# Kernel optimization log

Measured on AMD Instinct MI355X. Metric: run time of the kernel, lower is better.

## Reference

```python
import jax, jax.numpy as jnp
import numpy as np

B, S, D, H, DFF = 2, 2048, 2048, 16, 8192
DH = D // H
EPS = 1e-5


def _layer_norm(x, g, b):
    mu = jnp.mean(x, axis=-1, keepdims=True)
    var = jnp.mean(jnp.square(x - mu), axis=-1, keepdims=True)
    return (x - mu) * jax.lax.rsqrt(var + EPS) * g + b


def setup_inputs() -> dict:
    key = jax.random.key(0)
    ks = jax.random.split(key, 12)
    sc = 0.02
    inp = {
        "x": jax.random.normal(ks[0], (B, S, D), dtype=jnp.float32),
        # attention projections, stored [in, out] (torch Linear weight transposed)
        "wq": jax.random.normal(ks[1], (D, D), dtype=jnp.float32) * sc,
        "bq": jnp.zeros((D,), jnp.float32),
        "wk": jax.random.normal(ks[2], (D, D), dtype=jnp.float32) * sc,
        "bk": jnp.zeros((D,), jnp.float32),
        "wv": jax.random.normal(ks[3], (D, D), dtype=jnp.float32) * sc,
        "bv": jnp.zeros((D,), jnp.float32),
        "wo": jax.random.normal(ks[4], (D, D), dtype=jnp.float32) * sc,
        "bo": jnp.zeros((D,), jnp.float32),
        "ln1_g": jnp.ones((D,), jnp.float32),
        "ln1_b": jnp.zeros((D,), jnp.float32),
        # feed-forward
        "w1": jax.random.normal(ks[5], (D, DFF), dtype=jnp.float32) * sc,
        "b1": jnp.zeros((DFF,), jnp.float32),
        "w2": jax.random.normal(ks[6], (DFF, D), dtype=jnp.float32) * sc,
        "b2": jnp.zeros((D,), jnp.float32),
        "ln2_g": jnp.ones((D,), jnp.float32),
        "ln2_b": jnp.zeros((D,), jnp.float32),
    }
    return inp


def reference(x, wq, bq, wk, bk, wv, bv, wo, bo, ln1_g, ln1_b,
              w1, b1, w2, b2, ln2_g, ln2_b):
    # ---- MultiHeadAttentionBlock: x + MHA(LN(x)) ----
    h = _layer_norm(x, ln1_g, ln1_b)                      # [B,S,D]
    q = (h @ wq + bq).reshape(B, S, H, DH).transpose(0, 2, 1, 3)  # [B,H,S,DH]
    k = (h @ wk + bk).reshape(B, S, H, DH).transpose(0, 2, 1, 3)
    v = (h @ wv + bv).reshape(B, S, H, DH).transpose(0, 2, 1, 3)

    # faithful to source: scale by sqrt(d_dim), NOT sqrt(head_dim)
    scores = jnp.einsum("bhqd,bhkd->bhqk", q, k) / np.sqrt(D).astype(np.float32)
    # faithful triu/transpose masking (softmax sees raw zeros, not -inf)
    t = jnp.triu(scores).swapaxes(-2, -1)                 # [B,H,S,S]
    s = jax.nn.softmax(t, axis=-2)
    r = jnp.triu(s).swapaxes(-2, -1)
    attn = jnp.einsum("bhqk,bhkd->bhqd", r, v)            # [B,H,S,DH]
    attn = attn.transpose(0, 2, 1, 3).reshape(B, S, D)
    x = x + attn @ wo + bo

    # ---- FeedForwardBlock: x + FF(LN(x)), dropout rate 0 ----
    h2 = _layer_norm(x, ln2_g, ln2_b)
    ff = jax.nn.relu(h2 @ w1 + b1) @ w2 + b2
    return x + ff
```

## Files before the change

kernel.cpp:

```cpp
#include <hip/hip_runtime.h>


typedef unsigned short ushort_t;
typedef unsigned int   uint32;
typedef __attribute__((ext_vector_type(8))) short    short8;
typedef __attribute__((ext_vector_type(8))) ushort_t ushort8;
typedef __attribute__((ext_vector_type(4))) float    f32x4;

#define BDIM   2
#define SEQ    2048
#define DMODEL 2048
#define NHEAD  16
#define DHEAD  128
#define DFFN   8192
#define MROWS  (BDIM*SEQ)
#define LDQKV  6144

#define GPTR(p) (const __attribute__((address_space(1))) void*)((const void*)(p))
#define SPTR(p) (__attribute__((address_space(3))) void*)((void*)(p))

__device__ __forceinline__ float bf2f(ushort_t u) {
  union { uint32 i; float f; } c; c.i = ((uint32)u) << 16; return c.f;
}
__device__ __forceinline__ ushort_t f2bf(float f) {
  union { float f; uint32 i; } c; c.f = f;
  uint32 u = c.i;
  return (ushort_t)((u + 0x7fffu + ((u >> 16) & 1u)) >> 16);
}

__global__ __launch_bounds__(256) void transpose_f32_bf16_kern(
    const float* __restrict__ W, ushort_t* __restrict__ Wt, int K, int N)
{
  __shared__ float tile[32][33];
  const int nb = blockIdx.x * 32, kb = blockIdx.y * 32;
  const int tx = threadIdx.x & 31, ty = threadIdx.x >> 5;
#pragma unroll
  for (int j = 0; j < 32; j += 8)
    tile[ty + j][tx] = W[(size_t)(kb + ty + j) * N + nb + tx];
  __syncthreads();
#pragma unroll
  for (int j = 0; j < 32; j += 8)
    Wt[(size_t)(nb + ty + j) * K + kb + tx] = f2bf(tile[tx][ty + j]);
}

__global__ __launch_bounds__(256) void bias_concat_kern(
    const float* __restrict__ a, const float* __restrict__ b,
    const float* __restrict__ c, float* __restrict__ o)
{
  const int i = blockIdx.x * 256 + threadIdx.x;
  o[i] = (i < 2048) ? a[i] : ((i < 4096) ? b[i - 2048] : c[i - 4096]);
}

__global__ __launch_bounds__(256) void ln_kern(
    const float* __restrict__ X, const float* __restrict__ G,
    const float* __restrict__ Bb, ushort_t* __restrict__ Out)
{
  const int row = blockIdx.x, tid = threadIdx.x;
  const float* xr = X + (size_t)row * DMODEL;
  float4 v0 = ((const float4*)xr)[tid * 2];
  float4 v1 = ((const float4*)xr)[tid * 2 + 1];
  float s  = v0.x + v0.y + v0.z + v0.w + v1.x + v1.y + v1.z + v1.w;
  float ss = v0.x*v0.x + v0.y*v0.y + v0.z*v0.z + v0.w*v0.w
           + v1.x*v1.x + v1.y*v1.y + v1.z*v1.z + v1.w*v1.w;
#pragma unroll
  for (int off = 32; off > 0; off >>= 1) {
    s  += __shfl_down(s, off);
    ss += __shfl_down(ss, off);
  }
  __shared__ float rs[4], rss[4];
  __shared__ float sh_mu, sh_rst;
  const int wv = tid >> 6;
  if ((tid & 63) == 0) { rs[wv] = s; rss[wv] = ss; }
  __syncthreads();
  if (tid == 0) {
    float S1 = rs[0] + rs[1] + rs[2] + rs[3];
    float S2 = rss[0] + rss[1] + rss[2] + rss[3];
    float mu = S1 * (1.f / DMODEL);
    float var = S2 * (1.f / DMODEL) - mu * mu;
    sh_mu = mu;
    sh_rst = rsqrtf(var + 1e-5f);
  }
  __syncthreads();
  const float mu = sh_mu, rst = sh_rst;
  float4 g0 = ((const float4*)G)[tid * 2];
  float4 g1 = ((const float4*)G)[tid * 2 + 1];
  float4 b0 = ((const float4*)Bb)[tid * 2];
  float4 b1 = ((const float4*)Bb)[tid * 2 + 1];
  ushort8 o;
  o[0] = f2bf((v0.x - mu) * rst * g0.x + b0.x);
  o[1] = f2bf((v0.y - mu) * rst * g0.y + b0.y);
  o[2] = f2bf((v0.z - mu) * rst * g0.z + b0.z);
  o[3] = f2bf((v0.w - mu) * rst * g0.w + b0.w);
  o[4] = f2bf((v1.x - mu) * rst * g1.x + b1.x);
  o[5] = f2bf((v1.y - mu) * rst * g1.y + b1.y);
  o[6] = f2bf((v1.z - mu) * rst * g1.z + b1.z);
  o[7] = f2bf((v1.w - mu) * rst * g1.w + b1.w);
  *(ushort8*)(Out + (size_t)row * DMODEL + tid * 8) = o;
}

template<int OUT_BF16, int RELU, int RESID>
__global__ __launch_bounds__(512) void gemm_pipe_kern(
    const ushort_t* __restrict__ A, const ushort_t* __restrict__ Bt,
    const float* __restrict__ bias, const float* __restrict__ resid,
    void* __restrict__ Cout, int M, int N, int K)
{
  __shared__ ushort_t sA[3 * 128 * 64];
  __shared__ ushort_t sB[3 * 256 * 64];

  const int tid = threadIdx.x;
  const int nM  = gridDim.y;
  const int nwg = gridDim.x * nM;
  const int bid = blockIdx.y * gridDim.x + blockIdx.x;
  const int cpx = nwg >> 3;
  const int swz = (bid & 7) * cpx + (bid >> 3);
  const int m0 = (swz % nM) * 128;
  const int n0 = (swz / nM) * 256;

  const int l  = tid & 63, w = tid >> 6;
  const int lr = l & 15, lg = l >> 4;
  const int wr = w >> 2, wc = w & 3;

  const int srow  = tid >> 3;
  const int schunk = (tid & 7) ^ (srow & 7);
  const ushort_t* Asrc = A  + (size_t)(m0 + srow) * K + schunk * 8;
  const ushort_t* Bsrc = Bt + (size_t)(n0 + srow) * K + schunk * 8;
  ushort_t* sAd = sA + tid * 8;
  ushort_t* sBd = sB + tid * 8;

  const int rxk  = lr & 7;
  const int aoff = (wr * 64 + lr) * 64;
  const int boff = (wc * 64 + lr) * 64;

  f32x4 acc[4][4] = {};
  const int T = K >> 6;

#define STAGE_A(d, kt, r) __builtin_amdgcn_global_load_lds( \
    GPTR(Asrc + (size_t)(kt) * 64 + (size_t)(r) * 64 * K), \
    SPTR(sAd + (d) * 8192 + (r) * 4096), 16, 0, 0)
#define STAGE_B(d, kt, r) __builtin_amdgcn_global_load_lds( \
    GPTR(Bsrc + (size_t)(kt) * 64 + (size_t)(r) * 64 * K), \
    SPTR(sBd + (d) * 16384 + (r) * 4096), 16, 0, 0)

  STAGE_A(0, 0, 0); STAGE_A(0, 0, 1);
  STAGE_B(0, 0, 0); STAGE_B(0, 0, 1); STAGE_B(0, 0, 2); STAGE_B(0, 0, 3);
  STAGE_A(1, 1, 0); STAGE_A(1, 1, 1);
  STAGE_B(1, 1, 0); STAGE_B(1, 1, 1); STAGE_B(1, 1, 2); STAGE_B(1, 1, 3);
  asm volatile("s_waitcnt vmcnt(6)" ::: "memory");
  __builtin_amdgcn_s_barrier();
  __builtin_amdgcn_sched_barrier(0);

  int cur = 0;
  for (int t = 0; t < T; ++t) {
    const int nx = (cur == 0) ? 2 : cur - 1;
    const ushort_t* pA = sA + cur * 8192;
    const ushort_t* pB = sB + cur * 16384;
    const bool pf = (t + 2 < T);

    short8 a0 = *(const short8*)(pA + aoff +    0 + ((0 ^ rxk)) * 8 + (lg ^ 0) * 0);
    a0 = *(const short8*)(pA + aoff +    0 + ((lg ^ rxk)) * 8);
    short8 a1 = *(const short8*)(pA + aoff + 1024 + ((lg ^ rxk)) * 8);
    short8 a2 = *(const short8*)(pA + aoff + 2048 + ((lg ^ rxk)) * 8);
    short8 a3 = *(const short8*)(pA + aoff + 3072 + ((lg ^ rxk)) * 8);
    short8 b0 = *(const short8*)(pB + boff +    0 + ((lg ^ rxk)) * 8);
    short8 b1 = *(const short8*)(pB + boff + 1024 + ((lg ^ rxk)) * 8);
    short8 b2 = *(const short8*)(pB + boff + 2048 + ((lg ^ rxk)) * 8);
    short8 b3 = *(const short8*)(pB + boff + 3072 + ((lg ^ rxk)) * 8);
    if (pf) { STAGE_A(nx, t + 2, 0); STAGE_A(nx, t + 2, 1); STAGE_B(nx, t + 2, 0); }
    __builtin_amdgcn_s_barrier();
    asm volatile("s_waitcnt lgkmcnt(0)" ::: "memory");
    __builtin_amdgcn_sched_barrier(0);
    __builtin_amdgcn_s_setprio(1);
    acc[0][0] = __builtin_amdgcn_mfma_f32_16x16x32_bf16(a0, b0, acc[0][0], 0, 0, 0);
    acc[1][0] = __builtin_amdgcn_mfma_f32_16x16x32_bf16(a1, b0, acc[1][0], 0, 0, 0);
    acc[2][0] = __builtin_amdgcn_mfma_f32_16x16x32_bf16(a2, b0, acc[2][0], 0, 0, 0);
    acc[3][0] = __builtin_amdgcn_mfma_f32_16x16x32_bf16(a3, b0, acc[3][0], 0, 0, 0);
    acc[0][1] = __builtin_amdgcn_mfma_f32_16x16x32_bf16(a0, b1, acc[0][1], 0, 0, 0);
    acc[1][1] = __builtin_amdgcn_mfma_f32_16x16x32_bf16(a1, b1, acc[1][1], 0, 0, 0);
    acc[2][1] = __builtin_amdgcn_mfma_f32_16x16x32_bf16(a2, b1, acc[2][1], 0, 0, 0);
    acc[3][1] = __builtin_amdgcn_mfma_f32_16x16x32_bf16(a3, b1, acc[3][1], 0, 0, 0);
    acc[0][2] = __builtin_amdgcn_mfma_f32_16x16x32_bf16(a0, b2, acc[0][2], 0, 0, 0);
    acc[1][2] = __builtin_amdgcn_mfma_f32_16x16x32_bf16(a1, b2, acc[1][2], 0, 0, 0);
    acc[2][2] = __builtin_amdgcn_mfma_f32_16x16x32_bf16(a2, b2, acc[2][2], 0, 0, 0);
    acc[3][2] = __builtin_amdgcn_mfma_f32_16x16x32_bf16(a3, b2, acc[3][2], 0, 0, 0);
    acc[0][3] = __builtin_amdgcn_mfma_f32_16x16x32_bf16(a0, b3, acc[0][3], 0, 0, 0);
    acc[1][3] = __builtin_amdgcn_mfma_f32_16x16x32_bf16(a1, b3, acc[1][3], 0, 0, 0);
    acc[2][3] = __builtin_amdgcn_mfma_f32_16x16x32_bf16(a2, b3, acc[2][3], 0, 0, 0);
    acc[3][3] = __builtin_amdgcn_mfma_f32_16x16x32_bf16(a3, b3, acc[3][3], 0, 0, 0);
    __builtin_amdgcn_s_setprio(0);
    __builtin_amdgcn_s_barrier();

    a0 = *(const short8*)(pA + aoff +    0 + (((4 + lg) ^ rxk)) * 8);
    a1 = *(const short8*)(pA + aoff + 1024 + (((4 + lg) ^ rxk)) * 8);
    a2 = *(const short8*)(pA + aoff + 2048 + (((4 + lg) ^ rxk)) * 8);
    a3 = *(const short8*)(pA + aoff + 3072 + (((4 + lg) ^ rxk)) * 8);
    b0 = *(const short8*)(pB + boff +    0 + (((4 + lg) ^ rxk)) * 8);
    b1 = *(const short8*)(pB + boff + 1024 + (((4 + lg) ^ rxk)) * 8);
    b2 = *(const short8*)(pB + boff + 2048 + (((4 + lg) ^ rxk)) * 8);
    b3 = *(const short8*)(pB + boff + 3072 + (((4 + lg) ^ rxk)) * 8);
    if (pf) { STAGE_B(nx, t + 2, 1); STAGE_B(nx, t + 2, 2); STAGE_B(nx, t + 2, 3); }
    __builtin_amdgcn_s_barrier();
    asm volatile("s_waitcnt lgkmcnt(0)" ::: "memory");
    __builtin_amdgcn_sched_barrier(0);
    __builtin_amdgcn_s_setprio(1);
    acc[0][0] = __builtin_amdgcn_mfma_f32_16x16x32_bf16(a0, b0, acc[0][0], 0, 0, 0);
    acc[1][0] = __builtin_amdgcn_mfma_f32_16x16x32_bf16(a1, b0, acc[1][0], 0, 0, 0);
    acc[2][0] = __builtin_amdgcn_mfma_f32_16x16x32_bf16(a2, b0, acc[2][0], 0, 0, 0);
    acc[3][0] = __builtin_amdgcn_mfma_f32_16x16x32_bf16(a3, b0, acc[3][0], 0, 0, 0);
    acc[0][1] = __builtin_amdgcn_mfma_f32_16x16x32_bf16(a0, b1, acc[0][1], 0, 0, 0);
    acc[1][1] = __builtin_amdgcn_mfma_f32_16x16x32_bf16(a1, b1, acc[1][1], 0, 0, 0);
    acc[2][1] = __builtin_amdgcn_mfma_f32_16x16x32_bf16(a2, b1, acc[2][1], 0, 0, 0);
    acc[3][1] = __builtin_amdgcn_mfma_f32_16x16x32_bf16(a3, b1, acc[3][1], 0, 0, 0);
    acc[0][2] = __builtin_amdgcn_mfma_f32_16x16x32_bf16(a0, b2, acc[0][2], 0, 0, 0);
    acc[1][2] = __builtin_amdgcn_mfma_f32_16x16x32_bf16(a1, b2, acc[1][2], 0, 0, 0);
    acc[2][2] = __builtin_amdgcn_mfma_f32_16x16x32_bf16(a2, b2, acc[2][2], 0, 0, 0);
    acc[3][2] = __builtin_amdgcn_mfma_f32_16x16x32_bf16(a3, b2, acc[3][2], 0, 0, 0);
    acc[0][3] = __builtin_amdgcn_mfma_f32_16x16x32_bf16(a0, b3, acc[0][3], 0, 0, 0);
    acc[1][3] = __builtin_amdgcn_mfma_f32_16x16x32_bf16(a1, b3, acc[1][3], 0, 0, 0);
    acc[2][3] = __builtin_amdgcn_mfma_f32_16x16x32_bf16(a2, b3, acc[2][3], 0, 0, 0);
    acc[3][3] = __builtin_amdgcn_mfma_f32_16x16x32_bf16(a3, b3, acc[3][3], 0, 0, 0);
    __builtin_amdgcn_s_setprio(0);
    if (pf) { asm volatile("s_waitcnt vmcnt(6)" ::: "memory"); }
    else    { asm volatile("s_waitcnt vmcnt(0)" ::: "memory"); }
    __builtin_amdgcn_s_barrier();
    __builtin_amdgcn_sched_barrier(0);
    cur = (cur == 2) ? 0 : cur + 1;
  }
#undef STAGE_A
#undef STAGE_B

#pragma unroll
  for (int mi = 0; mi < 4; ++mi) {
#pragma unroll
    for (int ni = 0; ni < 4; ++ni) {
      const int gn = n0 + wc * 64 + ni * 16 + lr;
      const float bvv = bias[gn];
#pragma unroll
      for (int j = 0; j < 4; ++j) {
        const int gm = m0 + wr * 64 + mi * 16 + lg * 4 + j;
        float v = acc[mi][ni][j] + bvv;
        if (RESID) v += resid[(size_t)gm * N + gn];
        if (RELU) v = fmaxf(v, 0.f);
        if (OUT_BF16) ((ushort_t*)Cout)[(size_t)gm * N + gn] = f2bf(v);
        else          ((float*)Cout)[(size_t)gm * N + gn] = v;
      }
    }
  }
}

__global__ __launch_bounds__(256) void attn_stats_kern(
    const ushort_t* __restrict__ Q, const ushort_t* __restrict__ Kb,
    float* __restrict__ E, float* __restrict__ DG, int ld)
{
  __shared__ ushort_t Ksm[64 * 128];
  const int qb = blockIdx.x;
  const int bh = blockIdx.y;
  const int b = bh >> 4, h = bh & 15;
  const int tid = threadIdx.x;
  const int l = tid & 63, w = tid >> 6;
  const int lr = l & 15, lg = l >> 4;

  const int qrow0 = qb * 64 + w * 16;

  const size_t qoff = (size_t)(b * SEQ + qrow0 + lr) * ld + h * DHEAD + lg * 8;
  short8 af[4];
#pragma unroll
  for (int c = 0; c < 4; ++c) af[c] = *(const short8*)(Q + qoff + c * 32);

  const int srow_b = w * 16 + (l >> 4);
  const ushort_t* Kg = Kb + (size_t)b * SEQ * ld + (size_t)h * DHEAD;
  ushort_t* Sbase = Ksm + w * 2048;

  f32x4 sume = {0.f, 0.f, 0.f, 0.f};
  f32x4 dge  = {0.f, 0.f, 0.f, 0.f};
  const float scale = 0.0220970869120796f;
  const int rx = lr & 7;

  for (int kc = qb; kc < 32; ++kc) {
    __syncthreads();
#pragma unroll
    for (int c = 0; c < 4; ++c) {
      const int row = srow_b + c * 4;
      const int g = (l & 15) ^ (row & 7);
      __builtin_amdgcn_global_load_lds(
          GPTR(Kg + (size_t)(kc * 64 + row) * ld + g * 8),
          SPTR(Sbase + c * 512), 16, 0, 0);
    }
    __syncthreads();

    const int ks0 = (kc == qb) ? w : 0;
    for (int ks = ks0; ks < 4; ++ks) {
      short8 bfr[4];
#pragma unroll
      for (int c = 0; c < 4; ++c)
        bfr[c] = *(const short8*)(Ksm + (ks * 16 + lr) * 128 + ((lg + c * 4) ^ rx) * 8);
      f32x4 sc = {0.f, 0.f, 0.f, 0.f};
      sc = __builtin_amdgcn_mfma_f32_16x16x32_bf16(af[0], bfr[0], sc, 0, 0, 0);
      sc = __builtin_amdgcn_mfma_f32_16x16x32_bf16(af[1], bfr[1], sc, 0, 0, 0);
      sc = __builtin_amdgcn_mfma_f32_16x16x32_bf16(af[2], bfr[2], sc, 0, 0, 0);
      sc = __builtin_amdgcn_mfma_f32_16x16x32_bf16(af[3], bfr[3], sc, 0, 0, 0);
      if (kc == qb && ks == w) {
        const int ki = kc * 64 + ks * 16 + lr;
#pragma unroll
        for (int j = 0; j < 4; ++j) {
          const int qi = qrow0 + lg * 4 + j;
          if (ki >= qi) {
            float e = __expf(sc[j] * scale);
            sume[j] += e;
            if (ki == qi) dge[j] += e;
          }
        }
      } else {
#pragma unroll
        for (int j = 0; j < 4; ++j)
          sume[j] += __expf(sc[j] * scale);
      }
    }
  }

#pragma unroll
  for (int j = 0; j < 4; ++j) {
#pragma unroll
    for (int off = 1; off < 16; off <<= 1) {
      sume[j] += __shfl_xor(sume[j], off);
      dge[j]  += __shfl_xor(dge[j], off);
    }
  }
  if (lr == 0) {
#pragma unroll
    for (int j = 0; j < 4; ++j) {
      E[(size_t)bh * SEQ + qrow0 + lg * 4 + j]  = sume[j];
      DG[(size_t)bh * SEQ + qrow0 + lg * 4 + j] = dge[j];
    }
  }
}

__global__ __launch_bounds__(128) void vchunk_kern(
    const ushort_t* __restrict__ V, float* __restrict__ CS, int ld)
{
  const int c = blockIdx.x, bh = blockIdx.y;
  const int b = bh >> 4, h = bh & 15;
  const int dh = threadIdx.x;
  const ushort_t* vp = V + (size_t)(b * SEQ + c * 64) * ld + h * DHEAD + dh;
  float s = 0.f;
  for (int i = 0; i < 64; ++i) s += bf2f(vp[(size_t)i * ld]);
  CS[((size_t)bh * 32 + c) * 128 + dh] = s;
}

__global__ __launch_bounds__(128) void attn_combine_kern(
    const ushort_t* __restrict__ V, const float* __restrict__ CS,
    const float* __restrict__ E, const float* __restrict__ DG,
    ushort_t* __restrict__ Attn, int ldv)
{
  const int c = blockIdx.x, bh = blockIdx.y;
  const int b = bh >> 4, h = bh & 15;
  const int dh = threadIdx.x;
  float prefix = 0.f;
  for (int cc = 0; cc < c; ++cc) prefix += CS[((size_t)bh * 32 + cc) * 128 + dh];
  const ushort_t* vp = V + (size_t)(b * SEQ + c * 64) * ldv + h * DHEAD + dh;
  ushort_t* ap = Attn + (size_t)(b * SEQ + c * 64) * DMODEL + h * DHEAD + dh;
  const int qb = c * 64;
  for (int i = 0; i < 64; ++i) {
    const int qq = qb + i;
    const float denom = (float)qq + E[(size_t)bh * SEQ + qq];
    const float de = DG[(size_t)bh * SEQ + qq];
    const float vv = bf2f(vp[(size_t)i * ldv]);
    ap[(size_t)i * DMODEL] = f2bf((prefix + de * vv) / denom);
    prefix += vv;
  }
}

extern "C" void kernel_launch(void* const* d_in, const int* in_sizes, int n_in,
                              void* d_out, int out_size, void* d_ws, size_t ws_size,
                              hipStream_t stream)
{
  const float* x    = (const float*)d_in[0];
  const float* wq   = (const float*)d_in[1];
  const float* bq   = (const float*)d_in[2];
  const float* wk   = (const float*)d_in[3];
  const float* bk   = (const float*)d_in[4];
  const float* wv   = (const float*)d_in[5];
  const float* bv   = (const float*)d_in[6];
  const float* wo   = (const float*)d_in[7];
  const float* bo   = (const float*)d_in[8];
  const float* ln1g = (const float*)d_in[9];
  const float* ln1b = (const float*)d_in[10];
  const float* w1   = (const float*)d_in[11];
  const float* b1   = (const float*)d_in[12];
  const float* w2   = (const float*)d_in[13];
  const float* b2   = (const float*)d_in[14];
  const float* ln2g = (const float*)d_in[15];
  const float* ln2b = (const float*)d_in[16];
  float* out = (float*)d_out;

  char* ws = (char*)d_ws;
  ushort_t* W1T  = (ushort_t*)(ws + 0);
  ushort_t* W2T  = (ushort_t*)(ws + 33554432);
  ushort_t* WOT  = (ushort_t*)(ws + 67108864);
  float*    X2   = (float*)   (ws + 75497472);
  float*    Bcat = (float*)   (ws + 75497472);
  ushort_t* Hb   = (ushort_t*)(ws + 109051904);
  ushort_t* F1   = (ushort_t*)(ws + 125829120);
  ushort_t* WQKV = (ushort_t*)(ws + 125829120);
  ushort_t* QKVb = (ushort_t*)(ws + 150994944);
  float*    Eb   = (float*)   (ws + 201326592);
  float*    DGb  = (float*)   (ws + 201588736);
  float*    CSb  = (float*)   (ws + 201850880);

  transpose_f32_bf16_kern<<<dim3(64, 64),  256, 0, stream>>>(wq, WQKV,                 2048, 2048);
  transpose_f32_bf16_kern<<<dim3(64, 64),  256, 0, stream>>>(wk, WQKV + 2048 * 2048,   2048, 2048);
  transpose_f32_bf16_kern<<<dim3(64, 64),  256, 0, stream>>>(wv, WQKV + 2 * 2048 * 2048, 2048, 2048);
  transpose_f32_bf16_kern<<<dim3(64, 64),  256, 0, stream>>>(wo, WOT, 2048, 2048);
  transpose_f32_bf16_kern<<<dim3(256, 64), 256, 0, stream>>>(w1, W1T, 2048, 8192);
  transpose_f32_bf16_kern<<<dim3(64, 256), 256, 0, stream>>>(w2, W2T, 8192, 2048);
  bias_concat_kern<<<24, 256, 0, stream>>>(bq, bk, bv, Bcat);

  ln_kern<<<MROWS, 256, 0, stream>>>(x, ln1g, ln1b, Hb);

  gemm_pipe_kern<1, 0, 0><<<dim3(24, 32), 512, 0, stream>>>(Hb, WQKV, Bcat, nullptr, QKVb, MROWS, LDQKV, DMODEL);

  attn_stats_kern<<<dim3(32, 32), 256, 0, stream>>>(QKVb, QKVb + 2048, Eb, DGb, LDQKV);

  vchunk_kern<<<dim3(32, 32), 128, 0, stream>>>(QKVb + 4096, CSb, LDQKV);
  attn_combine_kern<<<dim3(32, 32), 128, 0, stream>>>(QKVb + 4096, CSb, Eb, DGb, Hb, LDQKV);

  gemm_pipe_kern<0, 0, 1><<<dim3(8, 32), 512, 0, stream>>>(Hb, WOT, bo, x, X2, MROWS, DMODEL, DMODEL);

  ln_kern<<<MROWS, 256, 0, stream>>>(X2, ln2g, ln2b, Hb);

  gemm_pipe_kern<1, 1, 0><<<dim3(32, 32), 512, 0, stream>>>(Hb, W1T, b1, nullptr, F1, MROWS, DFFN, DMODEL);

  gemm_pipe_kern<0, 0, 1><<<dim3(8, 32), 512, 0, stream>>>(F1, W2T, b2, X2, out, MROWS, DMODEL, DFFN);
}
```

Baseline: 719.6 us.

## Use 256x256 GEMM tiles with split-K partials and a combine kernel

Replaces the 128x256 triple-buffered GEMM with a 256x256 tile kernel that stages K in 32-wide half-slots across four LDS buffers, holding 8x4 accumulators per wave. The two N=2048 GEMMs (output projection and FFN down-projection) are split across K into two bf16 partial buffers, and a new combine kernel adds the partials, bias and residual. The goal is more data reuse per tile and enough workgroups on the narrow GEMMs to fill the device. In exchange it adds an extra elementwise pass, rounds partial sums to bf16, and raises register pressure.

After: 654.2 us. -9.1%, faster.

```diff
diff --git a/kernel.cpp b/kernel.cpp
--- a/kernel.cpp
+++ b/kernel.cpp
@@ -98,14 +98,14 @@
   *(ushort8*)(Out + (size_t)row * DMODEL + tid * 8) = o;
 }
 
-template<int OUT_BF16, int RELU, int RESID>
-__global__ __launch_bounds__(512) void gemm_pipe_kern(
+template<int OUT, int RELU, int RESID, int KDIV>
+__global__ __launch_bounds__(512, 2) void gemm8_kern(
     const ushort_t* __restrict__ A, const ushort_t* __restrict__ Bt,
     const float* __restrict__ bias, const float* __restrict__ resid,
     void* __restrict__ Cout, int M, int N, int K)
 {
-  __shared__ ushort_t sA[3 * 128 * 64];
-  __shared__ ushort_t sB[3 * 256 * 64];
+  __shared__ ushort_t sA[4 * 8192];
+  __shared__ ushort_t sB[4 * 8192];
 
   const int tid = threadIdx.x;
   const int nM  = gridDim.y;
@@ -113,138 +113,212 @@
   const int bid = blockIdx.y * gridDim.x + blockIdx.x;
   const int cpx = nwg >> 3;
   const int swz = (bid & 7) * cpx + (bid >> 3);
-  const int m0 = (swz % nM) * 128;
+  const int m0 = (swz % nM) * 256;
   const int n0 = (swz / nM) * 256;
 
-  const int l  = tid & 63, w = tid >> 6;
+  const int Keff = K / KDIV;
+  const int k0 = (KDIV > 1) ? blockIdx.z * Keff : 0;
+  const int T = Keff >> 6;
+
+  const int l = tid & 63, w = tid >> 6;
   const int lr = l & 15, lg = l >> 4;
   const int wr = w >> 2, wc = w & 3;
 
-  const int srow  = tid >> 3;
-  const int schunk = (tid & 7) ^ (srow & 7);
-  const ushort_t* Asrc = A  + (size_t)(m0 + srow) * K + schunk * 8;
-  const ushort_t* Bsrc = Bt + (size_t)(n0 + srow) * K + schunk * 8;
-  ushort_t* sAd = sA + tid * 8;
-  ushort_t* sBd = sB + tid * 8;
-
-  const int rxk  = lr & 7;
-  const int aoff = (wr * 64 + lr) * 64;
-  const int boff = (wc * 64 + lr) * 64;
-
-  f32x4 acc[4][4] = {};
-  const int T = K >> 6;
-
-#define STAGE_A(d, kt, r) __builtin_amdgcn_global_load_lds( \
-    GPTR(Asrc + (size_t)(kt) * 64 + (size_t)(r) * 64 * K), \
-    SPTR(sAd + (d) * 8192 + (r) * 4096), 16, 0, 0)
-#define STAGE_B(d, kt, r) __builtin_amdgcn_global_load_lds( \
-    GPTR(Bsrc + (size_t)(kt) * 64 + (size_t)(r) * 64 * K), \
-    SPTR(sBd + (d) * 16384 + (r) * 4096), 16, 0, 0)
-
-  STAGE_A(0, 0, 0); STAGE_A(0, 0, 1);
-  STAGE_B(0, 0, 0); STAGE_B(0, 0, 1); STAGE_B(0, 0, 2); STAGE_B(0, 0, 3);
-  STAGE_A(1, 1, 0); STAGE_A(1, 1, 1);
-  STAGE_B(1, 1, 0); STAGE_B(1, 1, 1); STAGE_B(1, 1, 2); STAGE_B(1, 1, 3);
-  asm volatile("s_waitcnt vmcnt(6)" ::: "memory");
+  const int xch   = (lg ^ ((lr >> 1) & 3)) * 8;
+  const int abase = (wr * 128 + lr) * 32 + xch;
+  const int bbase = (wc * 64  + lr) * 32 + xch;
+
+  const int sr = tid >> 2;
+  const int sg = ((tid & 3) ^ ((tid >> 3) & 3)) * 8;
+  const ushort_t* Asrc = A  + (size_t)(m0 + sr) * K + k0 + sg;
+  const ushort_t* Bsrc = Bt + (size_t)(n0 + sr) * K + k0 + sg;
+  ushort_t* dA = sA + tid * 8;
+  ushort_t* dB = sB + tid * 8;
+
+#define SA_(slot, kt, kk, r) __builtin_amdgcn_global_load_lds( \
+    GPTR(Asrc + (size_t)(r) * 128 * K + (kt) * 64 + (kk) * 32), \
+    SPTR(dA + (slot) * 8192 + (r) * 4096), 16, 0, 0)
+#define SB_(slot, kt, kk, r) __builtin_amdgcn_global_load_lds( \
+    GPTR(Bsrc + (size_t)(r) * 128 * K + (kt) * 64 + (kk) * 32), \
+    SPTR(dB + (slot) * 8192 + (r) * 4096), 16, 0, 0)
+
+  f32x4 acc[8][4] = {};
+
+  SA_(0, 0, 0, 0); SA_(0, 0, 0, 1); SB_(0, 0, 0, 0); SB_(0, 0, 0, 1);
+  SA_(1, 0, 1, 0); SA_(1, 0, 1, 1); SB_(1, 0, 1, 0); SB_(1, 0, 1, 1);
+  SA_(2, 1, 0, 0); SA_(2, 1, 0, 1); SB_(2, 1, 0, 0); SB_(2, 1, 0, 1);
+  asm volatile("s_waitcnt vmcnt(8)" ::: "memory");
   __builtin_amdgcn_s_barrier();
-  __builtin_amdgcn_sched_barrier(0);
-
-  int cur = 0;
+
   for (int t = 0; t < T; ++t) {
-    const int nx = (cur == 0) ? 2 : cur - 1;
-    const ushort_t* pA = sA + cur * 8192;
-    const ushort_t* pB = sB + cur * 16384;
-    const bool pf = (t + 2 < T);
-
-    short8 a0 = *(const short8*)(pA + aoff +    0 + ((0 ^ rxk)) * 8 + (lg ^ 0) * 0);
-    a0 = *(const short8*)(pA + aoff +    0 + ((lg ^ rxk)) * 8);
-    short8 a1 = *(const short8*)(pA + aoff + 1024 + ((lg ^ rxk)) * 8);
-    short8 a2 = *(const short8*)(pA + aoff + 2048 + ((lg ^ rxk)) * 8);
-    short8 a3 = *(const short8*)(pA + aoff + 3072 + ((lg ^ rxk)) * 8);
-    short8 b0 = *(const short8*)(pB + boff +    0 + ((lg ^ rxk)) * 8);
-    short8 b1 = *(const short8*)(pB + boff + 1024 + ((lg ^ rxk)) * 8);
-    short8 b2 = *(const short8*)(pB + boff + 2048 + ((lg ^ rxk)) * 8);
-    short8 b3 = *(const short8*)(pB + boff + 3072 + ((lg ^ rxk)) * 8);
-    if (pf) { STAGE_A(nx, t + 2, 0); STAGE_A(nx, t + 2, 1); STAGE_B(nx, t + 2, 0); }
-    __builtin_amdgcn_s_barrier();
-    asm volatile("s_waitcnt lgkmcnt(0)" ::: "memory");
-    __builtin_amdgcn_sched_barrier(0);
+    const int c = t & 1;
+    const ushort_t* A0 = sA + (c * 2 + 0) * 8192;
+    const ushort_t* B0 = sB + (c * 2 + 0) * 8192;
+    const ushort_t* A1 = sA + (c * 2 + 1) * 8192;
+    const ushort_t* B1 = sB + (c * 2 + 1) * 8192;
+    const int s1 = (c ^ 1) * 2 + 1;
+    const int s0 = c * 2;
+    const bool pf1 = (t + 1 < T), pf0 = (t + 2 < T);
+
+    short8 a0, a1, a2, a3, b0, b1, b2, b3;
+
+    b0 = *(const short8*)(B0 + bbase);
+    b1 = *(const short8*)(B0 + bbase + 512);
+    b2 = *(const short8*)(B0 + bbase + 1024);
+    b3 = *(const short8*)(B0 + bbase + 1536);
+    a0 = *(const short8*)(A0 + abase);
+    a1 = *(const short8*)(A0 + abase + 512);
+    a2 = *(const short8*)(A0 + abase + 1024);
+    a3 = *(const short8*)(A0 + abase + 1536);
+    if (pf1) { SA_(s1, t + 1, 1, 0); SA_(s1, t + 1, 1, 1); }
     __builtin_amdgcn_s_setprio(1);
     acc[0][0] = __builtin_amdgcn_mfma_f32_16x16x32_bf16(a0, b0, acc[0][0], 0, 0, 0);
+    acc[0][1] = __builtin_amdgcn_mfma_f32_16x16x32_bf16(a0, b1, acc[0][1], 0, 0, 0);
+    acc[0][2] = __builtin_amdgcn_mfma_f32_16x16x32_bf16(a0, b2, acc[0][2], 0, 0, 0);
+    acc[0][3] = __builtin_amdgcn_mfma_f32_16x16x32_bf16(a0, b3, acc[0][3], 0, 0, 0);
     acc[1][0] = __builtin_amdgcn_mfma_f32_16x16x32_bf16(a1, b0, acc[1][0], 0, 0, 0);
+    acc[1][1] = __builtin_amdgcn_mfma_f32_16x16x32_bf16(a1, b1, acc[1][1], 0, 0, 0);
+    acc[1][2] = __builtin_amdgcn_mfma_f32_16x16x32_bf16(a1, b2, acc[1][2], 0, 0, 0);
+    acc[1][3] = __builtin_amdgcn_mfma_f32_16x16x32_bf16(a1, b3, acc[1][3], 0, 0, 0);
     acc[2][0] = __builtin_amdgcn_mfma_f32_16x16x32_bf16(a2, b0, acc[2][0], 0, 0, 0);
+    acc[2][1] = __builtin_amdgcn_mfma_f32_16x16x32_bf16(a2, b1, acc[2][1], 0, 0, 0);
+    acc[2][2] = __builtin_amdgcn_mfma_f32_16x16x32_bf16(a2, b2, acc[2][2], 0, 0, 0);
+    acc[2][3] = __builtin_amdgcn_mfma_f32_16x16x32_bf16(a2, b3, acc[2][3], 0, 0, 0);
     acc[3][0] = __builtin_amdgcn_mfma_f32_16x16x32_bf16(a3, b0, acc[3][0], 0, 0, 0);
-    acc[0][1] = __builtin_amdgcn_mfma_f32_16x16x32_bf16(a0, b1, acc[0][1], 0, 0, 0);
-    acc[1][1] = __builtin_amdgcn_mfma_f32_16x16x32_bf16(a1, b1, acc[1][1], 0, 0, 0);
-    acc[2][1] = __builtin_amdgcn_mfma_f32_16x16x32_bf16(a2, b1, acc[2][1], 0, 0, 0);
     acc[3][1] = __builtin_amdgcn_mfma_f32_16x16x32_bf16(a3, b1, acc[3][1], 0, 0, 0);
-    acc[0][2] = __builtin_amdgcn_mfma_f32_16x16x32_bf16(a0, b2, acc[0][2], 0, 0, 0);
-    acc[1][2] = __builtin_amdgcn_mfma_f32_16x16x32_bf16(a1, b2, acc[1][2], 0, 0, 0);
-    acc[2][2] = __builtin_amdgcn_mfma_f32_16x16x32_bf16(a2, b2, acc[2][2], 0, 0, 0);
     acc[3][2] = __builtin_amdgcn_mfma_f32_16x16x32_bf16(a3, b2, acc[3][2], 0, 0, 0);
-    acc[0][3] = __builtin_amdgcn_mfma_f32_16x16x32_bf16(a0, b3, acc[0][3], 0, 0, 0);
-    acc[1][3] = __builtin_amdgcn_mfma_f32_16x16x32_bf16(a1, b3, acc[1][3], 0, 0, 0);
-    acc[2][3] = __builtin_amdgcn_mfma_f32_16x16x32_bf16(a2, b3, acc[2][3], 0, 0, 0);
     acc[3][3] = __builtin_amdgcn_mfma_f32_16x16x32_bf16(a3, b3, acc[3][3], 0, 0, 0);
     __builtin_amdgcn_s_setprio(0);
+
+    a0 = *(const short8*)(A0 + abase + 2048);
+    a1 = *(const short8*)(A0 + abase + 2560);
+    a2 = *(const short8*)(A0 + abase + 3072);
+    a3 = *(const short8*)(A0 + abase + 3584);
+    if (pf1) { SB_(s1, t + 1, 1, 0); SB_(s1, t + 1, 1, 1); }
+    __builtin_amdgcn_s_setprio(1);
+    acc[4][0] = __builtin_amdgcn_mfma_f32_16x16x32_bf16(a0, b0, acc[4][0], 0, 0, 0);
+    acc[4][1] = __builtin_amdgcn_mfma_f32_16x16x32_bf16(a0, b1, acc[4][1], 0, 0, 0);
+    acc[4][2] = __builtin_amdgcn_mfma_f32_16x16x32_bf16(a0, b2, acc[4][2], 0, 0, 0);
+    acc[4][3] = __builtin_amdgcn_mfma_f32_16x16x32_bf16(a0, b3, acc[4][3], 0, 0, 0);
+    acc[5][0] = __builtin_amdgcn_mfma_f32_16x16x32_bf16(a1, b0, acc[5][0], 0, 0, 0);
+    acc[5][1] = __builtin_amdgcn_mfma_f32_16x16x32_bf16(a1, b1, acc[5][1], 0, 0, 0);
+    acc[5][2] = __builtin_amdgcn_mfma_f32_16x16x32_bf16(a1, b2, acc[5][2], 0, 0, 0);
+    acc[5][3] = __builtin_amdgcn_mfma_f32_16x16x32_bf16(a1, b3, acc[5][3], 0, 0, 0);
+    acc[6][0] = __builtin_amdgcn_mfma_f32_16x16x32_bf16(a2, b0, acc[6][0], 0, 0, 0);
+    acc[6][1] = __builtin_amdgcn_mfma_f32_16x16x32_bf16(a2, b1, acc[6][1], 0, 0, 0);
+    acc[6][2] = __builtin_amdgcn_mfma_f32_16x16x32_bf16(a2, b2, acc[6][2], 0, 0, 0);
+    acc[6][3] = __builtin_amdgcn_mfma_f32_16x16x32_bf16(a2, b3, acc[6][3], 0, 0, 0);
+    acc[7][0] = __builtin_amdgcn_mfma_f32_16x16x32_bf16(a3, b0, acc[7][0], 0, 0, 0);
+    acc[7][1] = __builtin_amdgcn_mfma_f32_16x16x32_bf16(a3, b1, acc[7][1], 0, 0, 0);
+    acc[7][2] = __builtin_amdgcn_mfma_f32_16x16x32_bf16(a3, b2, acc[7][2], 0, 0, 0);
+    acc[7][3] = __builtin_amdgcn_mfma_f32_16x16x32_bf16(a3, b3, acc[7][3], 0, 0, 0);
+    __builtin_amdgcn_s_setprio(0);
+    if (t < T - 2) { asm volatile("s_waitcnt vmcnt(8)" ::: "memory"); }
+    else           { asm volatile("s_waitcnt vmcnt(0)" ::: "memory"); }
     __builtin_amdgcn_s_barrier();
 
-    a0 = *(const short8*)(pA + aoff +    0 + (((4 + lg) ^ rxk)) * 8);
-    a1 = *(const short8*)(pA + aoff + 1024 + (((4 + lg) ^ rxk)) * 8);
-    a2 = *(const short8*)(pA + aoff + 2048 + (((4 + lg) ^ rxk)) * 8);
-    a3 = *(const short8*)(pA + aoff + 3072 + (((4 + lg) ^ rxk)) * 8);
-    b0 = *(const short8*)(pB + boff +    0 + (((4 + lg) ^ rxk)) * 8);
-    b1 = *(const short8*)(pB + boff + 1024 + (((4 + lg) ^ rxk)) * 8);
-    b2 = *(const short8*)(pB + boff + 2048 + (((4 + lg) ^ rxk)) * 8);
-    b3 = *(const short8*)(pB + boff + 3072 + (((4 + lg) ^ rxk)) * 8);
-    if (pf) { STAGE_B(nx, t + 2, 1); STAGE_B(nx, t + 2, 2); STAGE_B(nx, t + 2, 3); }
-    __builtin_amdgcn_s_barrier();
-    asm volatile("s_waitcnt lgkmcnt(0)" ::: "memory");
-    __builtin_amdgcn_sched_barrier(0);
+    b0 = *(const short8*)(B1 + bbase);
+    b1 = *(const short8*)(B1 + bbase + 512);
+    b2 = *(const short8*)(B1 + bbase + 1024);
+    b3 = *(const short8*)(B1 + bbase + 1536);
+    a0 = *(const short8*)(A1 + abase);
+    a1 = *(const short8*)(A1 + abase + 512);
+    a2 = *(const short8*)(A1 + abase + 1024);
+    a3 = *(const short8*)(A1 + abase + 1536);
+    if (pf0) { SA_(s0, t + 2, 0, 0); SA_(s0, t + 2, 0, 1); }
     __builtin_amdgcn_s_setprio(1);
     acc[0][0] = __builtin_amdgcn_mfma_f32_16x16x32_bf16(a0, b0, acc[0][0], 0, 0, 0);
+    acc[0][1] = __builtin_amdgcn_mfma_f32_16x16x32_bf16(a0, b1, acc[0][1], 0, 0, 0);
+    acc[0][2] = __builtin_amdgcn_mfma_f32_16x16x32_bf16(a0, b2, acc[0][2], 0, 0, 0);
+    acc[0][3] = __builtin_amdgcn_mfma_f32_16x16x32_bf16(a0, b3, acc[0][3], 0, 0, 0);
     acc[1][0] = __builtin_amdgcn_mfma_f32_16x16x32_bf16(a1, b0, acc[1][0], 0, 0, 0);
+    acc[1][1] = __builtin_amdgcn_mfma_f32_16x16x32_bf16(a1, b1, acc[1][1], 0, 0, 0);
+    acc[1][2] = __builtin_amdgcn_mfma_f32_16x16x32_bf16(a1, b2, acc[1][2], 0, 0, 0);
+    acc[1][3] = __builtin_amdgcn_mfma_f32_16x16x32_bf16(a1, b3, acc[1][3], 0, 0, 0);
     acc[2][0] = __builtin_amdgcn_mfma_f32_16x16x32_bf16(a2, b0, acc[2][0], 0, 0, 0);
+    acc[2][1] = __builtin_amdgcn_mfma_f32_16x16x32_bf16(a2, b1, acc[2][1], 0, 0, 0);
+    acc[2][2] = __builtin_amdgcn_mfma_f32_16x16x32_bf16(a2, b2, acc[2][2], 0, 0, 0);
+    acc[2][3] = __builtin_amdgcn_mfma_f32_16x16x32_bf16(a2, b3, acc[2][3], 0, 0, 0);
     acc[3][0] = __builtin_amdgcn_mfma_f32_16x16x32_bf16(a3, b0, acc[3][0], 0, 0, 0);
-    acc[0][1] = __builtin_amdgcn_mfma_f32_16x16x32_bf16(a0, b1, acc[0][1], 0, 0, 0);
-    acc[1][1] = __builtin_amdgcn_mfma_f32_16x16x32_bf16(a1, b1, acc[1][1], 0, 0, 0);
-    acc[2][1] = __builtin_amdgcn_mfma_f32_16x16x32_bf16(a2, b1, acc[2][1], 0, 0, 0);
     acc[3][1] = __builtin_amdgcn_mfma_f32_16x16x32_bf16(a3, b1, acc[3][1], 0, 0, 0);
-    acc[0][2] = __builtin_amdgcn_mfma_f32_16x16x32_bf16(a0, b2, acc[0][2], 0, 0, 0);
-    acc[1][2] = __builtin_amdgcn_mfma_f32_16x16x32_bf16(a1, b2, acc[1][2], 0, 0, 0);
-    acc[2][2] = __builtin_amdgcn_mfma_f32_16x16x32_bf16(a2, b2, acc[2][2], 0, 0, 0);
     acc[3][2] = __builtin_amdgcn_mfma_f32_16x16x32_bf16(a3, b2, acc[3][2], 0, 0, 0);
-    acc[0][3] = __builtin_amdgcn_mfma_f32_16x16x32_bf16(a0, b3, acc[0][3], 0, 0, 0);
-    acc[1][3] = __builtin_amdgcn_mfma_f32_16x16x32_bf16(a1, b3, acc[1][3], 0, 0, 0);
-    acc[2][3] = __builtin_amdgcn_mfma_f32_16x16x32_bf16(a2, b3, acc[2][3], 0, 0, 0);
     acc[3][3] = __builtin_amdgcn_mfma_f32_16x16x32_bf16(a3, b3, acc[3][3], 0, 0, 0);
     __builtin_amdgcn_s_setprio(0);
-    if (pf) { asm volatile("s_waitcnt vmcnt(6)" ::: "memory"); }
-    else    { asm volatile("s_waitcnt vmcnt(0)" ::: "memory"); }
+
+    a0 = *(const short8*)(A1 + abase + 2048);
+    a1 = *(const short8*)(A1 + abase + 2560);
+    a2 = *(const short8*)(A1 + abase + 3072);
+    a3 = *(const short8*)(A1 + abase + 3584);
+    if (pf0) { SB_(s0, t + 2, 0, 0); SB_(s0, t + 2, 0, 1); }
+    __builtin_amdgcn_s_setprio(1);
+    acc[4][0] = __builtin_amdgcn_mfma_f32_16x16x32_bf16(a0, b0, acc[4][0], 0, 0, 0);
+    acc[4][1] = __builtin_amdgcn_mfma_f32_16x16x32_bf16(a0, b1, acc[4][1], 0, 0, 0);
+    acc[4][2] = __builtin_amdgcn_mfma_f32_16x16x32_bf16(a0, b2, acc[4][2], 0, 0, 0);
+    acc[4][3] = __builtin_amdgcn_mfma_f32_16x16x32_bf16(a0, b3, acc[4][3], 0, 0, 0);
+    acc[5][0] = __builtin_amdgcn_mfma_f32_16x16x32_bf16(a1, b0, acc[5][0], 0, 0, 0);
+    acc[5][1] = __builtin_amdgcn_mfma_f32_16x16x32_bf16(a1, b1, acc[5][1], 0, 0, 0);
+    acc[5][2] = __builtin_amdgcn_mfma_f32_16x16x32_bf16(a1, b2, acc[5][2], 0, 0, 0);
+    acc[5][3] = __builtin_amdgcn_mfma_f32_16x16x32_bf16(a1, b3, acc[5][3], 0, 0, 0);
+    acc[6][0] = __builtin_amdgcn_mfma_f32_16x16x32_bf16(a2, b0, acc[6][0], 0, 0, 0);
+    acc[6][1] = __builtin_amdgcn_mfma_f32_16x16x32_bf16(a2, b1, acc[6][1], 0, 0, 0);
+    acc[6][2] = __builtin_amdgcn_mfma_f32_16x16x32_bf16(a2, b2, acc[6][2], 0, 0, 0);
+    acc[6][3] = __builtin_amdgcn_mfma_f32_16x16x32_bf16(a2, b3, acc[6][3], 0, 0, 0);
+    acc[7][0] = __builtin_amdgcn_mfma_f32_16x16x32_bf16(a3, b0, acc[7][0], 0, 0, 0);
+    acc[7][1] = __builtin_amdgcn_mfma_f32_16x16x32_bf16(a3, b1, acc[7][1], 0, 0, 0);
+    acc[7][2] = __builtin_amdgcn_mfma_f32_16x16x32_bf16(a3, b2, acc[7][2], 0, 0, 0);
+    acc[7][3] = __builtin_amdgcn_mfma_f32_16x16x32_bf16(a3, b3, acc[7][3], 0, 0, 0);
+    __builtin_amdgcn_s_setprio(0);
+    if (t < T - 2) { asm volatile("s_waitcnt vmcnt(8)" ::: "memory"); }
+    else           { asm volatile("s_waitcnt vmcnt(0)" ::: "memory"); }
     __builtin_amdgcn_s_barrier();
-    __builtin_amdgcn_sched_barrier(0);
-    cur = (cur == 2) ? 0 : cur + 1;
-  }
-#undef STAGE_A
-#undef STAGE_B
-
-#pragma unroll
-  for (int mi = 0; mi < 4; ++mi) {
+  }
+#undef SA_
+#undef SB_
+
+  ushort_t* Pz = (OUT == 2)
+      ? (ushort_t*)Cout + (size_t)blockIdx.z * M * N : (ushort_t*)Cout;
+#pragma unroll
+  for (int mi = 0; mi < 8; ++mi) {
 #pragma unroll
     for (int ni = 0; ni < 4; ++ni) {
       const int gn = n0 + wc * 64 + ni * 16 + lr;
-      const float bvv = bias[gn];
+      const float bvv = (OUT == 2) ? 0.f : bias[gn];
 #pragma unroll
       for (int j = 0; j < 4; ++j) {
-        const int gm = m0 + wr * 64 + mi * 16 + lg * 4 + j;
+        const int gm = m0 + wr * 128 + mi * 16 + lg * 4 + j;
         float v = acc[mi][ni][j] + bvv;
         if (RESID) v += resid[(size_t)gm * N + gn];
         if (RELU) v = fmaxf(v, 0.f);
-        if (OUT_BF16) ((ushort_t*)Cout)[(size_t)gm * N + gn] = f2bf(v);
-        else          ((float*)Cout)[(size_t)gm * N + gn] = v;
+        if (OUT == 0)      ((float*)Cout)[(size_t)gm * N + gn] = v;
+        else               Pz[(size_t)gm * N + gn] = f2bf(v);
       }
     }
   }
+}
+
+__global__ __launch_bounds__(256) void combine_kern(
+    const ushort_t* __restrict__ pp, const float* __restrict__ bias,
+    const float* __restrict__ resid, float* __restrict__ out)
+{
+  const size_t i = ((size_t)blockIdx.x * 256 + threadIdx.x) * 8;
+  ushort8 p0 = *(const ushort8*)(pp + i);
+  ushort8 p1 = *(const ushort8*)(pp + (size_t)MROWS * 2048 + i);
+  const int col = (int)(i & 2047);
+  float4 r0 = *(const float4*)(resid + i);
+  float4 r1 = *(const float4*)(resid + i + 4);
+  float4 c0 = *(const float4*)(bias + col);
+  float4 c1 = *(const float4*)(bias + col + 4);
+  float4 o0, o1;
+  o0.x = bf2f(p0[0]) + bf2f(p1[0]) + c0.x + r0.x;
+  o0.y = bf2f(p0[1]) + bf2f(p1[1]) + c0.y + r0.y;
+  o0.z = bf2f(p0[2]) + bf2f(p1[2]) + c0.z + r0.z;
+  o0.w = bf2f(p0[3]) + bf2f(p1[3]) + c0.w + r0.w;
+  o1.x = bf2f(p0[4]) + bf2f(p1[4]) + c1.x + r1.x;
+  o1.y = bf2f(p0[5]) + bf2f(p1[5]) + c1.y + r1.y;
+  o1.z = bf2f(p0[6]) + bf2f(p1[6]) + c1.z + r1.z;
+  o1.w = bf2f(p0[7]) + bf2f(p1[7]) + c1.w + r1.w;
+  *(float4*)(out + i) = o0;
+  *(float4*)(out + i + 4) = o1;
 }
 
 __global__ __launch_bounds__(256) void attn_stats_kern(
@@ -394,20 +468,22 @@
 
   char* ws = (char*)d_ws;
   ushort_t* W1T  = (ushort_t*)(ws + 0);
+  ushort_t* PPf2 = (ushort_t*)(ws + 0);
   ushort_t* W2T  = (ushort_t*)(ws + 33554432);
   ushort_t* WOT  = (ushort_t*)(ws + 67108864);
   float*    X2   = (float*)   (ws + 75497472);
   float*    Bcat = (float*)   (ws + 75497472);
   ushort_t* Hb   = (ushort_t*)(ws + 109051904);
   ushort_t* F1   = (ushort_t*)(ws + 125829120);
+  ushort_t* PPwo = (ushort_t*)(ws + 125829120);
   ushort_t* WQKV = (ushort_t*)(ws + 125829120);
   ushort_t* QKVb = (ushort_t*)(ws + 150994944);
   float*    Eb   = (float*)   (ws + 201326592);
   float*    DGb  = (float*)   (ws + 201588736);
   float*    CSb  = (float*)   (ws + 201850880);
 
-  transpose_f32_bf16_kern<<<dim3(64, 64),  256, 0, stream>>>(wq, WQKV,                 2048, 2048);
-  transpose_f32_bf16_kern<<<dim3(64, 64),  256, 0, stream>>>(wk, WQKV + 2048 * 2048,   2048, 2048);
+  transpose_f32_bf16_kern<<<dim3(64, 64),  256, 0, stream>>>(wq, WQKV,                   2048, 2048);
+  transpose_f32_bf16_kern<<<dim3(64, 64),  256, 0, stream>>>(wk, WQKV + 2048 * 2048,     2048, 2048);
   transpose_f32_bf16_kern<<<dim3(64, 64),  256, 0, stream>>>(wv, WQKV + 2 * 2048 * 2048, 2048, 2048);
   transpose_f32_bf16_kern<<<dim3(64, 64),  256, 0, stream>>>(wo, WOT, 2048, 2048);
   transpose_f32_bf16_kern<<<dim3(256, 64), 256, 0, stream>>>(w1, W1T, 2048, 8192);
@@ -416,18 +492,24 @@
 
   ln_kern<<<MROWS, 256, 0, stream>>>(x, ln1g, ln1b, Hb);
 
-  gemm_pipe_kern<1, 0, 0><<<dim3(24, 32), 512, 0, stream>>>(Hb, WQKV, Bcat, nullptr, QKVb, MROWS, LDQKV, DMODEL);
+  gemm8_kern<1, 0, 0, 1><<<dim3(24, 16), 512, 0, stream>>>(
+      Hb, WQKV, Bcat, nullptr, QKVb, MROWS, LDQKV, DMODEL);
 
   attn_stats_kern<<<dim3(32, 32), 256, 0, stream>>>(QKVb, QKVb + 2048, Eb, DGb, LDQKV);
 
   vchunk_kern<<<dim3(32, 32), 128, 0, stream>>>(QKVb + 4096, CSb, LDQKV);
   attn_combine_kern<<<dim3(32, 32), 128, 0, stream>>>(QKVb + 4096, CSb, Eb, DGb, Hb, LDQKV);
 
-  gemm_pipe_kern<0, 0, 1><<<dim3(8, 32), 512, 0, stream>>>(Hb, WOT, bo, x, X2, MROWS, DMODEL, DMODEL);
+  gemm8_kern<2, 0, 0, 2><<<dim3(8, 16, 2), 512, 0, stream>>>(
+      Hb, WOT, bo, nullptr, PPwo, MROWS, DMODEL, DMODEL);
+  combine_kern<<<4096, 256, 0, stream>>>(PPwo, bo, x, X2);
 
   ln_kern<<<MROWS, 256, 0, stream>>>(X2, ln2g, ln2b, Hb);
 
-  gemm_pipe_kern<1, 1, 0><<<dim3(32, 32), 512, 0, stream>>>(Hb, W1T, b1, nullptr, F1, MROWS, DFFN, DMODEL);
-
-  gemm_pipe_kern<0, 0, 1><<<dim3(8, 32), 512, 0, stream>>>(F1, W2T, b2, X2, out, MROWS, DMODEL, DFFN);
-}
+  gemm8_kern<1, 1, 0, 1><<<dim3(32, 16), 512, 0, stream>>>(
+      Hb, W1T, b1, nullptr, F1, MROWS, DFFN, DMODEL);
+
+  gemm8_kern<2, 0, 0, 2><<<dim3(8, 16, 2), 512, 0, stream>>>(
+      F1, W2T, b2, nullptr, PPf2, MROWS, DMODEL, DFFN);
+  combine_kern<<<4096, 256, 0, stream>>>(PPf2, b2, X2, out);
+}
```
